# Kernel optimization log

Measured on AMD Instinct MI355X. Metric: run time of the kernel, lower is better.

## Reference

```python
import jax, jax.numpy as jnp
import numpy as np

E, D, H = 8, 512, 2048  # num_experts, features, features*mlp_ratio
B, S = 4, 512


def _lecun(key, shape):
    fan_in = shape[-2] if len(shape) >= 2 else shape[0]
    return jax.random.normal(key, shape, dtype=jnp.float32) / jnp.sqrt(jnp.float32(fan_in))


def setup_inputs() -> dict:
    key = jax.random.key(0)
    ks = jax.random.split(key, 8)
    return {
        'x_real': jax.random.normal(ks[0], (B, S, D), dtype=jnp.float32),
        'x_imag': jax.random.normal(ks[1], (B, S, D), dtype=jnp.float32),
        # gating Dense over concat([amp, phase]) -> in_features = 2*D
        'gate_W': _lecun(ks[2], (2 * D, E)),
        'gate_b': jnp.zeros((E,), jnp.float32),
        # per-expert ComplexLinear 1: D -> H
        'W1r': _lecun(ks[3], (E, D, H)),
        'W1i': _lecun(ks[4], (E, D, H)),
        'b1r': jnp.zeros((E, H), jnp.float32),
        'b1i': jnp.zeros((E, H), jnp.float32),
        # per-expert ComplexModReLU bias
        'mod_b': jnp.zeros((E, H), jnp.float32),
        # per-expert ComplexLinear 2: H -> D
        'W2r': _lecun(ks[5], (E, H, D)),
        'W2i': _lecun(ks[6], (E, H, D)),
        'b2r': jnp.zeros((E, D), jnp.float32),
        'b2i': jnp.zeros((E, D), jnp.float32),
    }


def reference(x_real, x_imag, gate_W, gate_b, W1r, W1i, b1r, b1i, mod_b, W2r, W2i, b2r, b2i):
    eps = 1e-10
    # --- gating: scores over [|z|, angle(z)] ---
    amp = jnp.sqrt(x_real ** 2 + x_imag ** 2)            # |z|, [B,S,D]
    phase = jnp.arctan2(x_imag, x_real)                  # angle(z)
    routing_input = jnp.concatenate([amp, phase], axis=-1)  # [B,S,2D]
    scores = routing_input @ gate_W + gate_b             # [B,S,E]
    probs = jax.nn.softmax(scores, axis=-1)
    idx = jnp.argmax(probs, axis=-1)                     # [B,S] top-1 expert

    # --- all experts dense (faithful to reference): complex linear 1 ---
    # (Wr + iWi)(xr + ixi) : hr = xr Wr - xi Wi ; hi = xr Wi + xi Wr
    h_r = (jnp.einsum('bsd,edh->ebsh', x_real, W1r)
           - jnp.einsum('bsd,edh->ebsh', x_imag, W1i)) + b1r[:, None, None, :]
    h_i = (jnp.einsum('bsd,edh->ebsh', x_real, W1i)
           + jnp.einsum('bsd,edh->ebsh', x_imag, W1r)) + b1i[:, None, None, :]

    # --- ComplexModReLU: relu(|z|+b) * z / (|z|+eps), |z| = sqrt(r^2+i^2+eps) ---
    a = jnp.sqrt(h_r ** 2 + h_i ** 2 + eps)              # [E,B,S,H]
    scale = jax.nn.relu(a + mod_b[:, None, None, :]) / (a + eps)
    h_r = h_r * scale
    h_i = h_i * scale

    # --- complex linear 2 ---
    o_r = (jnp.einsum('ebsh,ehd->ebsd', h_r, W2r)
           - jnp.einsum('ebsh,ehd->ebsd', h_i, W2i)) + b2r[:, None, None, :]
    o_i = (jnp.einsum('ebsh,ehd->ebsd', h_r, W2i)
           + jnp.einsum('ebsh,ehd->ebsd', h_i, W2r)) + b2i[:, None, None, :]

    # --- mask + weight (top-1): out = sum_e out_e * probs[...,e] * (argmax==e) ---
    e_ids = jnp.arange(probs.shape[-1])
    w = jnp.transpose(probs, (2, 0, 1)) * (idx[None, :, :] == e_ids[:, None, None])  # [E,B,S]
    out_r = jnp.einsum('ebs,ebsd->bsd', w, o_r)
    out_i = jnp.einsum('ebs,ebsd->bsd', w, o_i)
    return (out_r, out_i)
```

## Files before the change

### kernel.cpp

```cpp
#include <hip/hip_runtime.h>
#include <math.h>

#define NE 8
#define ND 512
#define NH 2048
#define NT 2048

typedef __attribute__((ext_vector_type(8))) short short8;
typedef __attribute__((ext_vector_type(4))) float f32x4;

#define GLL(g, d) __builtin_amdgcn_global_load_lds( \
    (const __attribute__((address_space(1))) void*)(g), \
    (__attribute__((address_space(3))) void*)(d), 16, 0, 0)

__device__ __forceinline__ unsigned short f2bf(float x) {
    unsigned int u = __builtin_bit_cast(unsigned int, x);
    u += 0x7FFFu + ((u >> 16) & 1u);
    return (unsigned short)(u >> 16);
}

__device__ __forceinline__ short8 neg8(short8 v) {
    int4 u = __builtin_bit_cast(int4, v);
    u.x ^= 0x80008000; u.y ^= 0x80008000; u.z ^= 0x80008000; u.w ^= 0x80008000;
    return __builtin_bit_cast(short8, u);
}

__device__ __forceinline__ short8 lds8(const unsigned short* p) {
    return *(const short8*)p;
}

__global__ __launch_bounds__(256) void gate_kernel(
    const float* __restrict__ xr, const float* __restrict__ xi,
    const float* __restrict__ gW, const float* __restrict__ gb,
    float* __restrict__ gate_w,
    int* __restrict__ counts, int* __restrict__ tok_list)
{
    int t = blockIdx.x;
    int tid = threadIdx.x;
    const float* xrt = xr + (size_t)t * ND;
    const float* xit = xi + (size_t)t * ND;

    float acc[NE] = {0,0,0,0,0,0,0,0};
    for (int r = tid; r < 2 * ND; r += 256) {
        int d = r & (ND - 1);
        float a = xrt[d], b = xit[d];
        float v = (r < ND) ? sqrtf(a * a + b * b) : atan2f(b, a);
        const float4* g = (const float4*)(gW + (size_t)r * NE);
        float4 g0 = g[0], g1 = g[1];
        acc[0] += v * g0.x; acc[1] += v * g0.y; acc[2] += v * g0.z; acc[3] += v * g0.w;
        acc[4] += v * g1.x; acc[5] += v * g1.y; acc[6] += v * g1.z; acc[7] += v * g1.w;
    }
    #pragma unroll
    for (int e = 0; e < NE; e++) {
        for (int off = 32; off > 0; off >>= 1)
            acc[e] += __shfl_down(acc[e], off, 64);
    }
    __shared__ float part[4][NE];
    int wave = tid >> 6, lane = tid & 63;
    if (lane == 0) {
        #pragma unroll
        for (int e = 0; e < NE; e++) part[wave][e] = acc[e];
    }
    __syncthreads();
    if (tid == 0) {
        float s[NE];
        #pragma unroll
        for (int e = 0; e < NE; e++)
            s[e] = part[0][e] + part[1][e] + part[2][e] + part[3][e] + gb[e];
        int amax = 0; float m = s[0];
        #pragma unroll
        for (int e = 1; e < NE; e++) if (s[e] > m) { m = s[e]; amax = e; }
        float denom = 0.f;
        #pragma unroll
        for (int e = 0; e < NE; e++) denom += expf(s[e] - m);
        gate_w[t] = 1.0f / denom;
        int pos = atomicAdd(&counts[amax], 1);
        tok_list[amax * NT + pos] = t;
    }
}

__global__ __launch_bounds__(256) void convx_kernel(
    const float* __restrict__ xr, const float* __restrict__ xi,
    unsigned short* __restrict__ obr, unsigned short* __restrict__ obi)
{
    int i = blockIdx.x * 256 + threadIdx.x;
    float4 vr = ((const float4*)xr)[i];
    float4 vi = ((const float4*)xi)[i];
    ((ushort4*)obr)[i] = make_ushort4(f2bf(vr.x), f2bf(vr.y), f2bf(vr.z), f2bf(vr.w));
    ((ushort4*)obi)[i] = make_ushort4(f2bf(vi.x), f2bf(vi.y), f2bf(vi.z), f2bf(vi.w));
}

__global__ __launch_bounds__(256) void transw_kernel(
    const float* __restrict__ s0, unsigned short* __restrict__ d0,
    const float* __restrict__ s1, unsigned short* __restrict__ d1,
    int R, int C)
{
    __shared__ float tile[64][65];
    int e = blockIdx.z;
    int c0 = blockIdx.x * 64, r0 = blockIdx.y * 64;
    size_t off = (size_t)e * R * C;
    int tid = threadIdx.x;
    #pragma unroll
    for (int p = 0; p < 2; ++p) {
        const float* src = (p ? s1 : s0) + off;
        unsigned short* dst = (p ? d1 : d0) + off;
        if (p) __syncthreads();
        for (int i = 0; i < 16; ++i) {
            int idx = tid + i * 256;
            int r = idx >> 6, c = idx & 63;
            tile[r][c] = src[(size_t)(r0 + r) * C + c0 + c];
        }
        __syncthreads();
        #pragma unroll
        for (int i = 0; i < 4; ++i) {
            int c = i * 16 + (tid >> 4);
            int r4 = (tid & 15) * 4;
            ushort4 v = make_ushort4(f2bf(tile[r4][c]), f2bf(tile[r4 + 1][c]),
                                     f2bf(tile[r4 + 2][c]), f2bf(tile[r4 + 3][c]));
            *(ushort4*)&dst[(size_t)(c0 + c) * R + r0 + r4] = v;
        }
    }
}


#define STAGE_(SA_R, SA_I, SB_R, SB_I, ko) do {  \
    GLL(gAr0 + (ko), SA_R + (w * 16) * 64);      \
    GLL(gAi0 + (ko), SA_I + (w * 16) * 64);      \
    GLL(gAr1 + (ko), SA_R + (w * 16 + 8) * 64);  \
    GLL(gAi1 + (ko), SA_I + (w * 16 + 8) * 64);  \
    GLL(gBr0 + (ko), SB_R + (w * 16) * 64);      \
    GLL(gBr1 + (ko), SB_R + (w * 16 + 8) * 64);  \
    GLL(gBi0 + (ko), SB_I + (w * 16) * 64);      \
    GLL(gBi1 + (ko), SB_I + (w * 16 + 8) * 64);  \
} while (0)

#define COMPUTE_(SA_R, SA_I, SB_R, SB_I) do {                                          \
    _Pragma("unroll")                                                                  \
    for (int ks = 0; ks < 2; ++ks) {                                                   \
        int pa = ((ks * 4 + quad) ^ (l15 & 7)) * 8;                                    \
        short8 br  = lds8(SB_R + (w * 16 + l15) * 64 + pa);                            \
        short8 bi2 = lds8(SB_I + (w * 16 + l15) * 64 + pa);                            \
        _Pragma("unroll")                                                              \
        for (int m = 0; m < 4; ++m) {                                                  \
            short8 ar  = lds8(SA_R + (m * 16 + l15) * 64 + pa);                        \
            short8 ai2 = lds8(SA_I + (m * 16 + l15) * 64 + pa);                        \
            short8 an  = neg8(ai2);                                                    \
            accr[m] = __builtin_amdgcn_mfma_f32_16x16x32_bf16(ar,  br,  accr[m], 0, 0, 0); \
            accr[m] = __builtin_amdgcn_mfma_f32_16x16x32_bf16(an,  bi2, accr[m], 0, 0, 0); \
            acci[m] = __builtin_amdgcn_mfma_f32_16x16x32_bf16(ar,  bi2, acci[m], 0, 0, 0); \
            acci[m] = __builtin_amdgcn_mfma_f32_16x16x32_bf16(ai2, br,  acci[m], 0, 0, 0); \
        }                                                                              \
    }                                                                                  \
} while (0)

#define SYNCPIPE do {                                               \
    asm volatile("s_waitcnt vmcnt(0) lgkmcnt(0)" ::: "memory");     \
    __builtin_amdgcn_s_barrier();                                   \
    __builtin_amdgcn_sched_barrier(0);                              \
} while (0)

#define MOE_LDS_DECL                                                        \
    __shared__ alignas(16) unsigned short sAr0[4096], sAi0[4096];           \
    __shared__ alignas(16) unsigned short sBr0[4096], sBi0[4096];           \
    __shared__ alignas(16) unsigned short sAr1[4096], sAi1[4096];           \
    __shared__ alignas(16) unsigned short sBr1[4096], sBi1[4096];

__global__ __launch_bounds__(256, 2) void moe1_kernel(
    const unsigned short* __restrict__ xbr, const unsigned short* __restrict__ xbi,
    const unsigned short* __restrict__ w1tr, const unsigned short* __restrict__ w1ti,
    const float* __restrict__ b1r, const float* __restrict__ b1i,
    const float* __restrict__ mod_b,
    const int* __restrict__ counts, const int* __restrict__ tok_list,
    unsigned short* __restrict__ hr, unsigned short* __restrict__ hi)
{
    int e = blockIdx.z;
    int n = counts[e];
    int mbase = blockIdx.y * 64;
    if (mbase >= n) return;
    int n0 = blockIdx.x * 64;
    int tid = threadIdx.x;
    int w = tid >> 6, l = tid & 63;
    int l15 = l & 15, quad = l >> 4;

    MOE_LDS_DECL

    const int* tl = tok_list + e * NT;
    int swz = (((l & 7) ^ ((l >> 3) & 7)) * 8);
    int ia0 = mbase + w * 16 + (l >> 3);
    int ia1 = ia0 + 8;
    int ra0 = tl[ia0 < n ? ia0 : n - 1];
    int ra1 = tl[ia1 < n ? ia1 : n - 1];
    const unsigned short* gAr0 = xbr + (size_t)ra0 * ND + swz;
    const unsigned short* gAi0 = xbi + (size_t)ra0 * ND + swz;
    const unsigned short* gAr1 = xbr + (size_t)ra1 * ND + swz;
    const unsigned short* gAi1 = xbi + (size_t)ra1 * ND + swz;
    size_t brow = (size_t)e * NH + n0 + w * 16 + (l >> 3);
    const unsigned short* gBr0 = w1tr + brow * ND + swz;
    const unsigned short* gBr1 = w1tr + (brow + 8) * ND + swz;
    const unsigned short* gBi0 = w1ti + brow * ND + swz;
    const unsigned short* gBi1 = w1ti + (brow + 8) * ND + swz;

    f32x4 accr[4] = {}, acci[4] = {};

    STAGE_(sAr0, sAi0, sBr0, sBi0, 0);
    SYNCPIPE;
    #pragma unroll 1
    for (int kt = 0; kt < ND / 64; kt += 2) {
        if (kt + 1 < ND / 64) STAGE_(sAr1, sAi1, sBr1, sBi1, (kt + 1) * 64);
        COMPUTE_(sAr0, sAi0, sBr0, sBi0);
        SYNCPIPE;
        if (kt + 2 < ND / 64) STAGE_(sAr0, sAi0, sBr0, sBi0, (kt + 2) * 64);
        COMPUTE_(sAr1, sAi1, sBr1, sBi1);
        SYNCPIPE;
    }

    int col = n0 + w * 16 + l15;
    float bre = b1r[(size_t)e * NH + col];
    float bie = b1i[(size_t)e * NH + col];
    float mbv = mod_b[(size_t)e * NH + col];
    #pragma unroll
    for (int m = 0; m < 4; ++m) {
        #pragma unroll
        for (int r = 0; r < 4; ++r) {
            int tix = m * 16 + quad * 4 + r;
            if (mbase + tix >= n) continue;
            int tok = tl[mbase + tix];
            float vr = accr[m][r] + bre;
            float vi = acci[m][r] + bie;
            float a = sqrtf(vr * vr + vi * vi + 1e-10f);
            float sc = fmaxf(a + mbv, 0.0f) / (a + 1e-10f);
            hr[(size_t)tok * NH + col] = f2bf(vr * sc);
            hi[(size_t)tok * NH + col] = f2bf(vi * sc);
        }
    }
}

__global__ __launch_bounds__(256, 2) void moe2_kernel(
    const unsigned short* __restrict__ hr, const unsigned short* __restrict__ hi,
    const unsigned short* __restrict__ w2tr, const unsigned short* __restrict__ w2ti,
    const float* __restrict__ b2r, const float* __restrict__ b2i,
    const int* __restrict__ counts, const int* __restrict__ tok_list,
    const float* __restrict__ gate_w,
    float* __restrict__ out)
{
    int e = blockIdx.z >> 1;
    int ksl = blockIdx.z & 1;
    int n = counts[e];
    int mbase = blockIdx.y * 64;
    if (mbase >= n) return;
    int n0 = blockIdx.x * 64;
    int kbase = ksl * (NH / 2);
    int tid = threadIdx.x;
    int w = tid >> 6, l = tid & 63;
    int l15 = l & 15, quad = l >> 4;

    MOE_LDS_DECL

    const int* tl = tok_list + e * NT;
    int swz = (((l & 7) ^ ((l >> 3) & 7)) * 8);
    int ia0 = mbase + w * 16 + (l >> 3);
    int ia1 = ia0 + 8;
    int ra0 = tl[ia0 < n ? ia0 : n - 1];
    int ra1 = tl[ia1 < n ? ia1 : n - 1];
    const unsigned short* gAr0 = hr + (size_t)ra0 * NH + kbase + swz;
    const unsigned short* gAi0 = hi + (size_t)ra0 * NH + kbase + swz;
    const unsigned short* gAr1 = hr + (size_t)ra1 * NH + kbase + swz;
    const unsigned short* gAi1 = hi + (size_t)ra1 * NH + kbase + swz;
    size_t brow = (size_t)e * ND + n0 + w * 16 + (l >> 3);
    const unsigned short* gBr0 = w2tr + brow * NH + kbase + swz;
    const unsigned short* gBr1 = w2tr + (brow + 8) * NH + kbase + swz;
    const unsigned short* gBi0 = w2ti + brow * NH + kbase + swz;
    const unsigned short* gBi1 = w2ti + (brow + 8) * NH + kbase + swz;

    f32x4 accr[4] = {}, acci[4] = {};

    STAGE_(sAr0, sAi0, sBr0, sBi0, 0);
    SYNCPIPE;
    #pragma unroll 1
    for (int kt = 0; kt < (NH / 2) / 64; kt += 2) {
        if (kt + 1 < (NH / 2) / 64) STAGE_(sAr1, sAi1, sBr1, sBi1, (kt + 1) * 64);
        COMPUTE_(sAr0, sAi0, sBr0, sBi0);
        SYNCPIPE;
        if (kt + 2 < (NH / 2) / 64) STAGE_(sAr0, sAi0, sBr0, sBi0, (kt + 2) * 64);
        COMPUTE_(sAr1, sAi1, sBr1, sBi1);
        SYNCPIPE;
    }

    int col = n0 + w * 16 + l15;
    float bre = (ksl == 0) ? b2r[(size_t)e * ND + col] : 0.0f;
    float bie = (ksl == 0) ? b2i[(size_t)e * ND + col] : 0.0f;
    #pragma unroll
    for (int m = 0; m < 4; ++m) {
        #pragma unroll
        for (int r = 0; r < 4; ++r) {
            int tix = m * 16 + quad * 4 + r;
            if (mbase + tix >= n) continue;
            int tok = tl[mbase + tix];
            float gw = gate_w[tok];
            atomicAdd(&out[(size_t)tok * ND + col], (accr[m][r] + bre) * gw);
            atomicAdd(&out[(size_t)NT * ND + (size_t)tok * ND + col], (acci[m][r] + bie) * gw);
        }
    }
}

extern "C" void kernel_launch(void* const* d_in, const int* in_sizes, int n_in,
                              void* d_out, int out_size, void* d_ws, size_t ws_size,
                              hipStream_t stream) {
    const float* xr   = (const float*)d_in[0];
    const float* xi   = (const float*)d_in[1];
    const float* gW   = (const float*)d_in[2];
    const float* gb   = (const float*)d_in[3];
    const float* W1r  = (const float*)d_in[4];
    const float* W1i  = (const float*)d_in[5];
    const float* b1r  = (const float*)d_in[6];
    const float* b1i  = (const float*)d_in[7];
    const float* modb = (const float*)d_in[8];
    const float* W2r  = (const float*)d_in[9];
    const float* W2i  = (const float*)d_in[10];
    const float* b2r  = (const float*)d_in[11];
    const float* b2i  = (const float*)d_in[12];
    float* out = (float*)d_out;

    char* ws = (char*)d_ws;
    int*   counts   = (int*)ws;
    float* gate_w   = (float*)(ws + 256);
    int*   tok_list = (int*)(ws + 256 + 8192);
    size_t off = 256 + 8192 + (size_t)NE * NT * 4;
    unsigned short* xbr  = (unsigned short*)(ws + off); off += (size_t)NT * ND * 2;
    unsigned short* xbi  = (unsigned short*)(ws + off); off += (size_t)NT * ND * 2;
    unsigned short* w1tr = (unsigned short*)(ws + off); off += (size_t)NE * ND * NH * 2;
    unsigned short* w1ti = (unsigned short*)(ws + off); off += (size_t)NE * ND * NH * 2;
    unsigned short* w2tr = (unsigned short*)(ws + off); off += (size_t)NE * ND * NH * 2;
    unsigned short* w2ti = (unsigned short*)(ws + off); off += (size_t)NE * ND * NH * 2;
    unsigned short* h_r  = (unsigned short*)(ws + off); off += (size_t)NT * NH * 2;
    unsigned short* h_i  = (unsigned short*)(ws + off); off += (size_t)NT * NH * 2;

    hipMemsetAsync(counts, 0, 64 * sizeof(int), stream);
    hipMemsetAsync(out, 0, (size_t)out_size * sizeof(float), stream);
    gate_kernel<<<NT, 256, 0, stream>>>(xr, xi, gW, gb, gate_w, counts, tok_list);
    convx_kernel<<<(NT * ND / 4) / 256, 256, 0, stream>>>(xr, xi, xbr, xbi);
    transw_kernel<<<dim3(NH / 64, ND / 64, NE), 256, 0, stream>>>(W1r, w1tr, W1i, w1ti, ND, NH);
    transw_kernel<<<dim3(ND / 64, NH / 64, NE), 256, 0, stream>>>(W2r, w2tr, W2i, w2ti, NH, ND);
    moe1_kernel<<<dim3(NH / 64, NT / 64, NE), 256, 0, stream>>>(
        xbr, xbi, w1tr, w1ti, b1r, b1i, modb, counts, tok_list, h_r, h_i);
    moe2_kernel<<<dim3(ND / 64, NT / 64, NE * 2), 256, 0, stream>>>(
        h_r, h_i, w2tr, w2ti, b2r, b2i, counts, tok_list, gate_w, out);
}
```

Baseline: 323.4 us.

## Split complex MFMA accumulators and overlap staging with compute via partial vmcnt waits

Replaces the two dependent-chain accumulators with four independent accumulators (RR, II, RI, IR), combined in the epilogue. This removes the per-step sign-flip of the imaginary A operand and breaks back-to-back MFMA dependencies on the same accumulator. The synchronisation is reworked so the next stage's global-to-LDS loads are issued before waiting only on the previous batch (vmcnt(8)), with barriers placed around compute. Doubling the accumulators raises register pressure, which may hurt the 2-blocks-per-CU occupancy.

```diff
diff --git a/kernel.cpp b/kernel.cpp
--- a/kernel.cpp
+++ b/kernel.cpp
@@ -17,12 +17,6 @@
     unsigned int u = __builtin_bit_cast(unsigned int, x);
     u += 0x7FFFu + ((u >> 16) & 1u);
     return (unsigned short)(u >> 16);
-}
-
-__device__ __forceinline__ short8 neg8(short8 v) {
-    int4 u = __builtin_bit_cast(int4, v);
-    u.x ^= 0x80008000; u.y ^= 0x80008000; u.z ^= 0x80008000; u.w ^= 0x80008000;
-    return __builtin_bit_cast(short8, u);
 }
 
 __device__ __forceinline__ short8 lds8(const unsigned short* p) {
@@ -144,19 +138,20 @@
         for (int m = 0; m < 4; ++m) {                                                  \
             short8 ar  = lds8(SA_R + (m * 16 + l15) * 64 + pa);                        \
             short8 ai2 = lds8(SA_I + (m * 16 + l15) * 64 + pa);                        \
-            short8 an  = neg8(ai2);                                                    \
-            accr[m] = __builtin_amdgcn_mfma_f32_16x16x32_bf16(ar,  br,  accr[m], 0, 0, 0); \
-            accr[m] = __builtin_amdgcn_mfma_f32_16x16x32_bf16(an,  bi2, accr[m], 0, 0, 0); \
-            acci[m] = __builtin_amdgcn_mfma_f32_16x16x32_bf16(ar,  bi2, acci[m], 0, 0, 0); \
-            acci[m] = __builtin_amdgcn_mfma_f32_16x16x32_bf16(ai2, br,  acci[m], 0, 0, 0); \
+            aRR[m] = __builtin_amdgcn_mfma_f32_16x16x32_bf16(ar,  br,  aRR[m], 0, 0, 0); \
+            aII[m] = __builtin_amdgcn_mfma_f32_16x16x32_bf16(ai2, bi2, aII[m], 0, 0, 0); \
+            aRI[m] = __builtin_amdgcn_mfma_f32_16x16x32_bf16(ar,  bi2, aRI[m], 0, 0, 0); \
+            aIR[m] = __builtin_amdgcn_mfma_f32_16x16x32_bf16(ai2, br,  aIR[m], 0, 0, 0); \
         }                                                                              \
     }                                                                                  \
 } while (0)
 
-#define SYNCPIPE do {                                               \
-    asm volatile("s_waitcnt vmcnt(0) lgkmcnt(0)" ::: "memory");     \
-    __builtin_amdgcn_s_barrier();                                   \
-    __builtin_amdgcn_sched_barrier(0);                              \
+#define VMW8  asm volatile("s_waitcnt vmcnt(8)" ::: "memory")
+#define VMW0  asm volatile("s_waitcnt vmcnt(0)" ::: "memory")
+#define BARX do {                            \
+    __builtin_amdgcn_sched_barrier(0);       \
+    __builtin_amdgcn_s_barrier();            \
+    __builtin_amdgcn_sched_barrier(0);       \
 } while (0)
 
 #define MOE_LDS_DECL                                                        \
@@ -164,6 +159,24 @@
     __shared__ alignas(16) unsigned short sBr0[4096], sBi0[4096];           \
     __shared__ alignas(16) unsigned short sAr1[4096], sAi1[4096];           \
     __shared__ alignas(16) unsigned short sBr1[4096], sBi1[4096];
+
+#define PIPE_LOOP(NK) do {                                                  \
+    STAGE_(sAr0, sAi0, sBr0, sBi0, 0);                                      \
+    VMW0; BARX;                                                             \
+    _Pragma("unroll 1")                                                     \
+    for (int kt = 0; kt < (NK); kt += 2) {                                  \
+        if (kt + 1 < (NK)) { STAGE_(sAr1, sAi1, sBr1, sBi1, (kt + 1) * 64); VMW8; } \
+        else VMW0;                                                          \
+        BARX;                                                               \
+        COMPUTE_(sAr0, sAi0, sBr0, sBi0);                                   \
+        BARX;                                                               \
+        if (kt + 2 < (NK)) { STAGE_(sAr0, sAi0, sBr0, sBi0, (kt + 2) * 64); VMW8; } \
+        else VMW0;                                                          \
+        BARX;                                                               \
+        COMPUTE_(sAr1, sAi1, sBr1, sBi1);                                   \
+        BARX;                                                               \
+    }                                                                       \
+} while (0)
 
 __global__ __launch_bounds__(256, 2) void moe1_kernel(
     const unsigned short* __restrict__ xbr, const unsigned short* __restrict__ xbi,
@@ -200,19 +213,9 @@
     const unsigned short* gBi0 = w1ti + brow * ND + swz;
     const unsigned short* gBi1 = w1ti + (brow + 8) * ND + swz;
 
-    f32x4 accr[4] = {}, acci[4] = {};
-
-    STAGE_(sAr0, sAi0, sBr0, sBi0, 0);
-    SYNCPIPE;
-    #pragma unroll 1
-    for (int kt = 0; kt < ND / 64; kt += 2) {
-        if (kt + 1 < ND / 64) STAGE_(sAr1, sAi1, sBr1, sBi1, (kt + 1) * 64);
-        COMPUTE_(sAr0, sAi0, sBr0, sBi0);
-        SYNCPIPE;
-        if (kt + 2 < ND / 64) STAGE_(sAr0, sAi0, sBr0, sBi0, (kt + 2) * 64);
-        COMPUTE_(sAr1, sAi1, sBr1, sBi1);
-        SYNCPIPE;
-    }
+    f32x4 aRR[4] = {}, aII[4] = {}, aRI[4] = {}, aIR[4] = {};
+
+    PIPE_LOOP(ND / 64);
 
     int col = n0 + w * 16 + l15;
     float bre = b1r[(size_t)e * NH + col];
@@ -225,8 +228,8 @@
             int tix = m * 16 + quad * 4 + r;
             if (mbase + tix >= n) continue;
             int tok = tl[mbase + tix];
-            float vr = accr[m][r] + bre;
-            float vi = acci[m][r] + bie;
+            float vr = aRR[m][r] - aII[m][r] + bre;
+            float vi = aRI[m][r] + aIR[m][r] + bie;
             float a = sqrtf(vr * vr + vi * vi + 1e-10f);
             float sc = fmaxf(a + mbv, 0.0f) / (a + 1e-10f);
             hr[(size_t)tok * NH + col] = f2bf(vr * sc);
@@ -272,19 +275,9 @@
     const unsigned short* gBi0 = w2ti + brow * NH + kbase + swz;
     const unsigned short* gBi1 = w2ti + (brow + 8) * NH + kbase + swz;
 
-    f32x4 accr[4] = {}, acci[4] = {};
-
-    STAGE_(sAr0, sAi0, sBr0, sBi0, 0);
-    SYNCPIPE;
-    #pragma unroll 1
-    for (int kt = 0; kt < (NH / 2) / 64; kt += 2) {
-        if (kt + 1 < (NH / 2) / 64) STAGE_(sAr1, sAi1, sBr1, sBi1, (kt + 1) * 64);
-        COMPUTE_(sAr0, sAi0, sBr0, sBi0);
-        SYNCPIPE;
-        if (kt + 2 < (NH / 2) / 64) STAGE_(sAr0, sAi0, sBr0, sBi0, (kt + 2) * 64);
-        COMPUTE_(sAr1, sAi1, sBr1, sBi1);
-        SYNCPIPE;
-    }
+    f32x4 aRR[4] = {}, aII[4] = {}, aRI[4] = {}, aIR[4] = {};
+
+    PIPE_LOOP((NH / 2) / 64);
 
     int col = n0 + w * 16 + l15;
     float bre = (ksl == 0) ? b2r[(size_t)e * ND + col] : 0.0f;
@@ -297,8 +290,8 @@
             if (mbase + tix >= n) continue;
             int tok = tl[mbase + tix];
             float gw = gate_w[tok];
-            atomicAdd(&out[(size_t)tok * ND + col], (accr[m][r] + bre) * gw);
-            atomicAdd(&out[(size_t)NT * ND + (size_t)tok * ND + col], (acci[m][r] + bie) * gw);
+            atomicAdd(&out[(size_t)tok * ND + col], (aRR[m][r] - aII[m][r] + bre) * gw);
+            atomicAdd(&out[(size_t)NT * ND + (size_t)tok * ND + col], (aRI[m][r] + aIR[m][r] + bie) * gw);
         }
     }
 }
```

After: 319.0 us. About the same (-1.4%).
